# Optimization experiments

Measured on AMD Instinct MI355X. Metric: run time of the kernel, lower is better.

## Reference

```python
import jax, jax.numpy as jnp
import numpy as np

B, T, D, H, DH, FF = 512, 64, 512, 8, 64, 2048
SCALE = DH ** -0.5  # head_dim ** -0.5


def _ln(x, g, b):
    m = x.mean(-1, keepdims=True)
    v = x.var(-1, keepdims=True)
    return (x - m) / jnp.sqrt(v + 1e-5) * g + b


def _l2n(x):
    return x / jnp.maximum(jnp.linalg.norm(x, axis=-1, keepdims=True), 1e-12)


def setup_inputs() -> dict:
    key = jax.random.key(0)
    ks = jax.random.split(key, 16)

    def w(k, shape):
        fan_in = shape[0]
        return jax.random.normal(k, shape, jnp.float32) / np.sqrt(fan_in).astype(np.float32)

    return {
        'item_seq': jax.random.normal(ks[0], (B, T, D), jnp.float32),
        'user_static_emb': jax.random.normal(ks[1], (B, D), jnp.float32),
        'last_item_emb': jax.random.normal(ks[2], (B, D), jnp.float32),
        'init_state': jnp.zeros((B, H, DH, DH), jnp.float32),
        'Wq': w(ks[3], (D, D)), 'Wk': w(ks[4], (D, D)), 'Wv': w(ks[5], (D, D)),
        'Wa': w(ks[6], (D, H)), 'ba': jnp.zeros((H,), jnp.float32),
        'We': w(ks[7], (D, H)), 'be': jnp.zeros((H,), jnp.float32),
        'mcW1': w(ks[8], (2 * D, D)), 'mcb1': jnp.zeros((D,), jnp.float32),
        'mcg': jnp.ones((D,), jnp.float32), 'mcbt': jnp.zeros((D,), jnp.float32),
        'mcW2': w(ks[9], (D, 2 * D + 2 * H)), 'mcb2': jnp.zeros((2 * D + 2 * H,), jnp.float32),
        'Wo': w(ks[10], (D, D)), 'bo': jnp.zeros((D,), jnp.float32),
        'W1': w(ks[11], (D, FF)), 'b1': jnp.zeros((FF,), jnp.float32),
        'W2': w(ks[12], (FF, D)), 'b2': jnp.zeros((D,), jnp.float32),
        'n1g': jnp.ones((D,), jnp.float32), 'n1b': jnp.zeros((D,), jnp.float32),
        'n2g': jnp.ones((D,), jnp.float32), 'n2b': jnp.zeros((D,), jnp.float32),
    }


def reference(item_seq, user_static_emb, last_item_emb, init_state,
              Wq, Wk, Wv, Wa, ba, We, be,
              mcW1, mcb1, mcg, mcbt, mcW2, mcb2,
              Wo, bo, W1, b1, W2, b2, n1g, n1b, n2g, n2b):
    def read(q_emb, state):
        # q: (B,H,Dh) L2-normalized; read = S @ q per head
        q = _l2n((q_emb @ Wq).reshape(-1, H, DH))
        return jnp.einsum('bhij,bhj->bhi', state, q).reshape(-1, D)

    us_norm = _ln(user_static_emb, n1g, n1b)  # constant across steps

    def step(state, item):
        i_norm = _ln(item, n1g, n1b)
        mem_ctx = read(i_norm, state)
        meta_in = jnp.concatenate([us_norm, mem_ctx], axis=-1)
        h = jax.nn.relu(_ln(meta_in @ mcW1 + mcb1, mcg, mcbt))
        mo = h @ mcW2 + mcb2
        gamma, beta = mo[:, :D], mo[:, D:2 * D]
        alpha_bias, eta_bias = mo[:, 2 * D:2 * D + H], mo[:, 2 * D + H:]
        mod = i_norm * (1.0 + jnp.tanh(gamma)) + beta
        k = _l2n((mod @ Wk).reshape(-1, H, DH))
        v = (mod @ Wv).reshape(-1, H, DH)
        alpha = jax.nn.sigmoid(mod @ Wa + ba + alpha_bias)[:, :, None, None]
        eta = (jax.nn.sigmoid(mod @ We + be + eta_bias) * SCALE)[:, :, None, None]
        pred = jnp.einsum('bhij,bhj->bhi', state, k)
        upd = jnp.einsum('bhi,bhj->bhij', v - pred, k)  # rank-1 outer-product write
        return (1.0 - alpha) * state + eta * upd, None

    state, _ = jax.lax.scan(step, init_state, jnp.swapaxes(item_seq, 0, 1))

    # predict (read) path
    q_norm = _ln(last_item_emb, n1g, n1b)
    attn = read(q_norm, state) @ Wo + bo
    x = user_static_emb + attn
    x2 = _ln(x, n2g, n2b)
    ffn = jax.nn.relu(x2 @ W1 + b1) @ W2 + b2
    return x + ffn
```

## Files before the change

kernel.cpp:

```cpp
#include <hip/hip_runtime.h>
#include <cmath>

constexpr int cB = 512, cT = 64, cD = 512, cH = 8, cDH = 64, cFF = 2048;
constexpr float cSCALE = 0.125f;

typedef short bfrag __attribute__((ext_vector_type(8)));
typedef float f32x4 __attribute__((ext_vector_type(4)));

__device__ __forceinline__ short f2bf(float x) {
  union { float f; unsigned u; } v{x};
  unsigned r = v.u + 0x7fff + ((v.u >> 16) & 1);
  return (short)(r >> 16);
}
__device__ __forceinline__ float bf2f(short s) {
  union { unsigned u; float f; } v;
  v.u = ((unsigned)(unsigned short)s) << 16;
  return v.f;
}
__device__ __forceinline__ float sigm(float z) { return 1.f / (1.f + __expf(-z)); }

enum GemmMode { MQ = 0, MWO, MFF1, MFF2 };

struct GemmArgs {
  const float *A, *A2, *sm, *sr, *g, *b;
  const short *WT, *WT2;
  const float *bias, *extra;
  float *O;
  short *Os;
};

template<int MODE>
__device__ __forceinline__ float loadA(const GemmArgs& p, int r, int k) {
  if constexpr (MODE == MQ) {
    int t = r >> 9, bb = r & 511;
    float v = (t < cT) ? p.A[((size_t)bb * cT + t) * cD + k]
                       : p.A2[(size_t)bb * cD + k];
    return (v - p.sm[r]) * p.sr[r] * p.g[k] + p.b[k];
  } else if constexpr (MODE == MFF1) {
    return (p.A[(size_t)r * cD + k] - p.sm[r]) * p.sr[r] * p.g[k] + p.b[k];
  } else if constexpr (MODE == MFF2) {
    return p.A[(size_t)r * cFF + k];
  } else {
    return p.A[(size_t)r * cD + k];
  }
}

template<int MODE>
__device__ __forceinline__ void epi(const GemmArgs& p, int r, int cn, float acc) {
  if constexpr (MODE == MQ) {
    p.Os[(size_t)r * cD + cn] = f2bf(acc);
  } else if constexpr (MODE == MWO) {
    p.O[(size_t)r * cD + cn] = p.extra[(size_t)r * cD + cn] + acc + p.bias[cn];
  } else if constexpr (MODE == MFF1) {
    p.O[(size_t)r * cFF + cn] = fmaxf(acc + p.bias[cn], 0.f);
  } else {
    p.O[(size_t)r * cD + cn] = p.extra[(size_t)r * cD + cn] + acc + p.bias[cn];
  }
}

template<int MODE, int LDW>
__global__ __launch_bounds__(256) void mgemm(GemmArgs p, int K) {
  __shared__ short As[64][32];
  __shared__ short Bs[64][32];
  const int tid = threadIdx.x;
  const int lane = tid & 63, wid = tid >> 6;
  const int wm = wid & 1, wn = wid >> 1;
  const int l15 = lane & 15, qd = lane >> 4;
  const int row0 = blockIdx.x * 64;
  const int n0 = blockIdx.y * 64;

  f32x4 acc[2][2] = {};
  const int sm = tid >> 2;
  const int sk = (tid & 3) * 8;

  for (int k0 = 0; k0 < K; k0 += 32) {
    {
      short tmp[8];
#pragma unroll
      for (int j = 0; j < 8; ++j)
        tmp[j] = f2bf(loadA<MODE>(p, row0 + sm, k0 + sk + j));
      *((bfrag*)&As[sm][0] + (sk >> 3)) = *(bfrag*)tmp;
    }
    *((bfrag*)&Bs[sm][0] + (sk >> 3)) =
        *(const bfrag*)(p.WT + (size_t)(n0 + sm) * LDW + k0 + sk);
    __syncthreads();
    bfrag a0 = *((bfrag*)&As[wm * 32 + l15][0] + qd);
    bfrag a1 = *((bfrag*)&As[wm * 32 + 16 + l15][0] + qd);
    bfrag b0 = *((bfrag*)&Bs[wn * 32 + l15][0] + qd);
    bfrag b1 = *((bfrag*)&Bs[wn * 32 + 16 + l15][0] + qd);
    acc[0][0] = __builtin_amdgcn_mfma_f32_16x16x32_bf16(a0, b0, acc[0][0], 0, 0, 0);
    acc[0][1] = __builtin_amdgcn_mfma_f32_16x16x32_bf16(a0, b1, acc[0][1], 0, 0, 0);
    acc[1][0] = __builtin_amdgcn_mfma_f32_16x16x32_bf16(a1, b0, acc[1][0], 0, 0, 0);
    acc[1][1] = __builtin_amdgcn_mfma_f32_16x16x32_bf16(a1, b1, acc[1][1], 0, 0, 0);
    __syncthreads();
  }

#pragma unroll
  for (int fm = 0; fm < 2; ++fm)
#pragma unroll
    for (int fn = 0; fn < 2; ++fn)
#pragma unroll
      for (int rg = 0; rg < 4; ++rg)
        epi<MODE>(p, row0 + wm * 32 + fm * 16 + qd * 4 + rg,
                  n0 + wn * 32 + fn * 16 + l15, acc[fm][fn][rg]);
}

template<int MODE, int LDW>
__global__ __launch_bounds__(256) void pgemm(GemmArgs p, int K) {
  __shared__ short Ah[64][32], Al[64][32];
  __shared__ short Bh[64][32], Bl[64][32];
  const int tid = threadIdx.x;
  const int lane = tid & 63, wid = tid >> 6;
  const int wm = wid & 1, wn = wid >> 1;
  const int l15 = lane & 15, qd = lane >> 4;
  const int row0 = blockIdx.x * 64;
  const int n0 = blockIdx.y * 64;

  f32x4 acc[2][2] = {};
  const int sm = tid >> 2;
  const int sk = (tid & 3) * 8;

  for (int k0 = 0; k0 < K; k0 += 32) {
    {
      short th[8], tl[8];
#pragma unroll
      for (int j = 0; j < 8; ++j) {
        float a = loadA<MODE>(p, row0 + sm, k0 + sk + j);
        short h = f2bf(a);
        th[j] = h;
        tl[j] = f2bf(a - bf2f(h));
      }
      *((bfrag*)&Ah[sm][0] + (sk >> 3)) = *(bfrag*)th;
      *((bfrag*)&Al[sm][0] + (sk >> 3)) = *(bfrag*)tl;
    }
    *((bfrag*)&Bh[sm][0] + (sk >> 3)) =
        *(const bfrag*)(p.WT + (size_t)(n0 + sm) * LDW + k0 + sk);
    *((bfrag*)&Bl[sm][0] + (sk >> 3)) =
        *(const bfrag*)(p.WT2 + (size_t)(n0 + sm) * LDW + k0 + sk);
    __syncthreads();
#pragma unroll
    for (int fm = 0; fm < 2; ++fm) {
      bfrag ah = *((bfrag*)&Ah[wm * 32 + fm * 16 + l15][0] + qd);
      bfrag al = *((bfrag*)&Al[wm * 32 + fm * 16 + l15][0] + qd);
#pragma unroll
      for (int fn = 0; fn < 2; ++fn) {
        bfrag bh = *((bfrag*)&Bh[wn * 32 + fn * 16 + l15][0] + qd);
        bfrag bl = *((bfrag*)&Bl[wn * 32 + fn * 16 + l15][0] + qd);
        acc[fm][fn] = __builtin_amdgcn_mfma_f32_16x16x32_bf16(al, bh, acc[fm][fn], 0, 0, 0);
        acc[fm][fn] = __builtin_amdgcn_mfma_f32_16x16x32_bf16(ah, bl, acc[fm][fn], 0, 0, 0);
        acc[fm][fn] = __builtin_amdgcn_mfma_f32_16x16x32_bf16(ah, bh, acc[fm][fn], 0, 0, 0);
      }
    }
    __syncthreads();
  }

#pragma unroll
  for (int fm = 0; fm < 2; ++fm)
#pragma unroll
    for (int fn = 0; fn < 2; ++fn)
#pragma unroll
      for (int rg = 0; rg < 4; ++rg)
        epi<MODE>(p, row0 + wm * 32 + fm * 16 + qd * 4 + rg,
                  n0 + wn * 32 + fn * 16 + l15, acc[fm][fn][rg]);
}

__global__ __launch_bounds__(256) void tconv(const float* __restrict__ W,
                                             short* __restrict__ WT, int K, int N) {
  __shared__ float tile[32][33];
  int k0 = blockIdx.x * 32, n0 = blockIdx.y * 32;
  int tx = threadIdx.x & 31, ty = threadIdx.x >> 5;
#pragma unroll
  for (int j = 0; j < 32; j += 8) {
    int k = k0 + ty + j, n = n0 + tx;
    tile[ty + j][tx] = (k < K && n < N) ? W[(size_t)k * N + n] : 0.f;
  }
  __syncthreads();
#pragma unroll
  for (int j = 0; j < 32; j += 8) {
    int n = n0 + ty + j, k = k0 + tx;
    if (n < N && k < K) WT[(size_t)n * K + k] = f2bf(tile[tx][ty + j]);
  }
}

__global__ __launch_bounds__(256) void tconv2(const float* __restrict__ W,
                                              short* __restrict__ WTh,
                                              short* __restrict__ WTl, int K, int N) {
  __shared__ float tile[32][33];
  int k0 = blockIdx.x * 32, n0 = blockIdx.y * 32;
  int tx = threadIdx.x & 31, ty = threadIdx.x >> 5;
#pragma unroll
  for (int j = 0; j < 32; j += 8) {
    int k = k0 + ty + j, n = n0 + tx;
    tile[ty + j][tx] = (k < K && n < N) ? W[(size_t)k * N + n] : 0.f;
  }
  __syncthreads();
#pragma unroll
  for (int j = 0; j < 32; j += 8) {
    int n = n0 + ty + j, k = k0 + tx;
    if (n < N && k < K) {
      float v = tile[tx][ty + j];
      short h = f2bf(v);
      WTh[(size_t)n * K + k] = h;
      WTl[(size_t)n * K + k] = f2bf(v - bf2f(h));
    }
  }
}

__global__ __launch_bounds__(256) void ln_stats_k(
    const float* __restrict__ item_seq, const float* __restrict__ last_item,
    const float* __restrict__ user, const float* __restrict__ n1g,
    const float* __restrict__ n1b, float* __restrict__ lnm,
    float* __restrict__ lnr, float* __restrict__ us_norm) {
  const int lane = threadIdx.x & 63;
  const int w = blockIdx.x * 4 + (threadIdx.x >> 6);
  const float* src;
  int cls, bi = 0;
  if (w < cT * cB) {
    int t = w >> 9, bb = w & 511;
    src = item_seq + ((size_t)bb * cT + t) * cD;
    cls = 0;
  } else if (w < cT * cB + cB) {
    bi = w - cT * cB;
    src = last_item + (size_t)bi * cD;
    cls = 1;
  } else {
    bi = w - cT * cB - cB;
    src = user + (size_t)bi * cD;
    cls = 2;
  }
  float x[8], s = 0.f, ss = 0.f;
#pragma unroll
  for (int i = 0; i < 8; ++i) {
    float v = src[lane + i * 64];
    x[i] = v; s += v; ss += v * v;
  }
#pragma unroll
  for (int o = 32; o >= 1; o >>= 1) { s += __shfl_xor(s, o); ss += __shfl_xor(ss, o); }
  float m = s * (1.f / cD);
  float rstd = rsqrtf(ss * (1.f / cD) - m * m + 1e-5f);
  if (cls == 0) {
    if (lane == 0) { lnm[w] = m; lnr[w] = rstd; }
  } else if (cls == 1) {
    if (lane == 0) { lnm[cT * cB + bi] = m; lnr[cT * cB + bi] = rstd; }
  } else {
#pragma unroll
    for (int i = 0; i < 8; ++i) {
      int d = lane + i * 64;
      us_norm[(size_t)bi * cD + d] = (x[i] - m) * rstd * n1g[d] + n1b[d];
    }
  }
}

__global__ __launch_bounds__(256) void row_stats_k(const float* __restrict__ X,
                                                   float* __restrict__ M,
                                                   float* __restrict__ R) {
  const int lane = threadIdx.x & 63;
  const int w = blockIdx.x * 4 + (threadIdx.x >> 6);
  float s = 0.f, ss = 0.f;
#pragma unroll
  for (int i = 0; i < 8; ++i) {
    float v = X[(size_t)w * cD + lane + i * 64];
    s += v; ss += v * v;
  }
#pragma unroll
  for (int o = 32; o >= 1; o >>= 1) { s += __shfl_xor(s, o); ss += __shfl_xor(ss, o); }
  if (lane == 0) {
    float m = s * (1.f / cD);
    M[w] = m;
    R[w] = rsqrtf(ss * (1.f / cD) - m * m + 1e-5f);
  }
}

struct Scan2Params {
  const float *item_seq, *init_state, *us_norm, *lnm, *lnr, *n1g, *n1b;
  const float *mcb1, *mcg, *mcbt, *mcb2, *ba, *be;
  const short *wt_m1, *wt_m2, *wt_k, *wt_v, *wt_ae, *q_all;
  float *mem_ctx;
};

__device__ __forceinline__ bfrag mk_afrag(const float* xr, int kc, int qd) {
  const float* s = xr + kc * 32 + qd * 8;
  float4 a = *(const float4*)s;
  float4 b = *(const float4*)(s + 4);
  short t[8] = {f2bf(a.x), f2bf(a.y), f2bf(a.z), f2bf(a.w),
                f2bf(b.x), f2bf(b.y), f2bf(b.z), f2bf(b.w)};
  return *(bfrag*)t;
}

__global__ __launch_bounds__(1024, 4) void scan2_k(Scan2Params p) {
  const int tid = threadIdx.x;
  const int lane = tid & 63, w = tid >> 6;
  const int bb = w >> 3, h = w & 7;
  const int l15 = lane & 15, qd = lane >> 4;
  const int b0 = blockIdx.x * 2;

  __shared__ float xcat[2][1024];
  __shared__ float rbuf[2][512];
  __shared__ float x2b[2][512];
  __shared__ float mo[2][1040];
  __shared__ float modv[2][512];
  __shared__ float kvb[2][1024];
  __shared__ float khat[16][64];
  __shared__ float qh[16][64];
  __shared__ float aeta[2][8][2];
  __shared__ float st[2][2], st2[2][2];
  __shared__ float cb1[512], cg[512], cbt[512], cb2[1040];
  __shared__ float cn1g[512], cn1b[512], cba[8], cbe[8];

  if (tid < 512) {
    cb1[tid] = p.mcb1[tid]; cg[tid] = p.mcg[tid]; cbt[tid] = p.mcbt[tid];
    cn1g[tid] = p.n1g[tid]; cn1b[tid] = p.n1b[tid];
  }
  cb2[tid] = p.mcb2[tid];
  if (tid < 16) cb2[1024 + tid] = p.mcb2[1024 + tid];
  if (tid < 8) { cba[tid] = p.ba[tid]; cbe[tid] = p.be[tid]; }
  {
    int row = tid >> 9, c = tid & 511;
    xcat[row][c] = p.us_norm[(size_t)(b0 + row) * cD + c];
  }

  float S[64];
  {
    const float* sp = p.init_state + ((((size_t)(b0 + bb)) * cH + h) * cDH + lane) * cDH;
#pragma unroll
    for (int j = 0; j < 64; j += 4) {
      float4 t4 = *(const float4*)(sp + j);
      S[j] = t4.x; S[j + 1] = t4.y; S[j + 2] = t4.z; S[j + 3] = t4.w;
    }
  }
  float memv;
  {
    float qv = bf2f(p.q_all[(size_t)(b0 + bb) * cD + h * cDH + lane]);
    float qs = qv * qv;
#pragma unroll
    for (int o = 32; o >= 1; o >>= 1) qs += __shfl_xor(qs, o);
    qh[w][lane] = qv / fmaxf(sqrtf(qs), 1e-12f);
    memv = 0.f;
#pragma unroll
    for (int j = 0; j < 64; j += 4) {
      float4 q4 = *(const float4*)&qh[w][j];
      memv += S[j] * q4.x + S[j + 1] * q4.y + S[j + 2] * q4.z + S[j + 3] * q4.w;
    }
    xcat[bb][512 + h * cDH + lane] = memv;
  }
  __syncthreads();

  for (int t = 0; t < cT; ++t) {
    {
      f32x4 a0 = {}, a1 = {};
      const int n0 = w * 16, n1 = (w + 16) * 16;
#pragma unroll 4
      for (int kc = 0; kc < 32; ++kc) {
        bfrag A = {};
        if (l15 < 2) A = mk_afrag(&xcat[l15][0], kc, qd);
        bfrag B0 = *(const bfrag*)(p.wt_m1 + (size_t)(n0 + l15) * 1024 + kc * 32 + qd * 8);
        bfrag B1 = *(const bfrag*)(p.wt_m1 + (size_t)(n1 + l15) * 1024 + kc * 32 + qd * 8);
        a0 = __builtin_amdgcn_mfma_f32_16x16x32_bf16(A, B0, a0, 0, 0, 0);
        a1 = __builtin_amdgcn_mfma_f32_16x16x32_bf16(A, B1, a1, 0, 0, 0);
      }
      if (lane < 16) {
        rbuf[0][n0 + lane] = a0[0] + cb1[n0 + lane];
        rbuf[1][n0 + lane] = a0[1] + cb1[n0 + lane];
        rbuf[0][n1 + lane] = a1[0] + cb1[n1 + lane];
        rbuf[1][n1 + lane] = a1[1] + cb1[n1 + lane];
      }
    }
    __syncthreads();
    if (w < 2) {
      float s = 0.f, ss = 0.f;
#pragma unroll
      for (int i = 0; i < 8; ++i) { float v = rbuf[w][lane + i * 64]; s += v; ss += v * v; }
#pragma unroll
      for (int o = 32; o >= 1; o >>= 1) { s += __shfl_xor(s, o); ss += __shfl_xor(ss, o); }
      if (lane == 0) {
        float m = s * (1.f / cD);
        st[w][0] = m;
        st[w][1] = rsqrtf(ss * (1.f / cD) - m * m + 1e-5f);
      }
    } else if (w == 2 && lane < 2) {
      st2[lane][0] = p.lnm[t * cB + b0 + lane];
      st2[lane][1] = p.lnr[t * cB + b0 + lane];
    }
    __syncthreads();
    {
      int row = tid >> 9, c = tid & 511;
      x2b[row][c] = fmaxf((rbuf[row][c] - st[row][0]) * st[row][1] * cg[c] + cbt[c], 0.f);
    }
    __syncthreads();
    {
      f32x4 acc[4] = {};
#pragma unroll 2
      for (int kc = 0; kc < 16; ++kc) {
        bfrag A = {};
        if (l15 < 2) A = mk_afrag(&x2b[l15][0], kc, qd);
#pragma unroll
        for (int tI = 0; tI < 4; ++tI) {
          int n0 = (tI * 16 + w) * 16;
          bfrag B = *(const bfrag*)(p.wt_m2 + (size_t)(n0 + l15) * 512 + kc * 32 + qd * 8);
          acc[tI] = __builtin_amdgcn_mfma_f32_16x16x32_bf16(A, B, acc[tI], 0, 0, 0);
        }
      }
      if (lane < 16)
#pragma unroll
        for (int tI = 0; tI < 4; ++tI) {
          int n0 = (tI * 16 + w) * 16;
          mo[0][n0 + lane] = acc[tI][0] + cb2[n0 + lane];
          mo[1][n0 + lane] = acc[tI][1] + cb2[n0 + lane];
        }
      if (w == 0) {
        f32x4 e = {};
        for (int kc = 0; kc < 16; ++kc) {
          bfrag A = {};
          if (l15 < 2) A = mk_afrag(&x2b[l15][0], kc, qd);
          bfrag B = *(const bfrag*)(p.wt_m2 + (size_t)(1024 + l15) * 512 + kc * 32 + qd * 8);
          e = __builtin_amdgcn_mfma_f32_16x16x32_bf16(A, B, e, 0, 0, 0);
        }
        if (lane < 16) {
          mo[0][1024 + lane] = e[0] + cb2[1024 + lane];
          mo[1][1024 + lane] = e[1] + cb2[1024 + lane];
        }
      }
    }
    __syncthreads();
    {
      int row = tid >> 9, c = tid & 511;
      float inm = (p.item_seq[(((size_t)(b0 + row)) * cT + t) * cD + c] - st2[row][0]) *
                      st2[row][1] * cn1g[c] + cn1b[c];
      modv[row][c] = inm * (1.f + tanhf(mo[row][c])) + mo[row][512 + c];
    }
    __syncthreads();
    {
      f32x4 acc[4] = {};
#pragma unroll 2
      for (int kc = 0; kc < 16; ++kc) {
        bfrag A = {};
        if (l15 < 2) A = mk_afrag(&modv[l15][0], kc, qd);
#pragma unroll
        for (int tI = 0; tI < 4; ++tI) {
          int tile = tI * 16 + w;
          const short* wt = (tile < 32) ? p.wt_k : p.wt_v;
          int n0 = ((tile < 32) ? tile : tile - 32) * 16;
          bfrag B = *(const bfrag*)(wt + (size_t)(n0 + l15) * 512 + kc * 32 + qd * 8);
          acc[tI] = __builtin_amdgcn_mfma_f32_16x16x32_bf16(A, B, acc[tI], 0, 0, 0);
        }
      }
      if (lane < 16)
#pragma unroll
        for (int tI = 0; tI < 4; ++tI) {
          int tile = tI * 16 + w;
          int dst = (tile < 32) ? tile * 16 + lane : 512 + (tile - 32) * 16 + lane;
          kvb[0][dst] = acc[tI][0];
          kvb[1][dst] = acc[tI][1];
        }
      if (w == 0) {
        f32x4 e = {};
        for (int kc = 0; kc < 16; ++kc) {
          bfrag A = {};
          if (l15 < 2) A = mk_afrag(&modv[l15][0], kc, qd);
          bfrag B = *(const bfrag*)(p.wt_ae + (size_t)l15 * 512 + kc * 32 + qd * 8);
          e = __builtin_amdgcn_mfma_f32_16x16x32_bf16(A, B, e, 0, 0, 0);
        }
        if (lane < 16) {
          if (lane < 8) {
            int hh = lane;
            aeta[0][hh][0] = sigm(e[0] + cba[hh] + mo[0][1024 + hh]);
            aeta[1][hh][0] = sigm(e[1] + cba[hh] + mo[1][1024 + hh]);
          } else {
            int hh = lane - 8;
            aeta[0][hh][1] = cSCALE * sigm(e[0] + cbe[hh] + mo[0][1032 + hh]);
            aeta[1][hh][1] = cSCALE * sigm(e[1] + cbe[hh] + mo[1][1032 + hh]);
          }
        }
      }
    }
    __syncthreads();
    {
      float kvv = kvb[bb][h * cDH + lane];
      float ks = kvv * kvv;
#pragma unroll
      for (int o = 32; o >= 1; o >>= 1) ks += __shfl_xor(ks, o);
      khat[w][lane] = kvv / fmaxf(sqrtf(ks), 1e-12f);
      float qv = bf2f(p.q_all[((size_t)(t + 1) * cB + (b0 + bb)) * cD + h * cDH + lane]);
      float qs = qv * qv;
#pragma unroll
      for (int o = 32; o >= 1; o >>= 1) qs += __shfl_xor(qs, o);
      qh[w][lane] = qv / fmaxf(sqrtf(qs), 1e-12f);

      float vv = kvb[bb][512 + h * cDH + lane];
      float al = aeta[bb][h][0], et = aeta[bb][h][1];
      float pred = 0.f;
#pragma unroll
      for (int j = 0; j < 64; j += 4) {
        float4 k4 = *(const float4*)&khat[w][j];
        pred += S[j] * k4.x + S[j + 1] * k4.y + S[j + 2] * k4.z + S[j + 3] * k4.w;
      }
      float f = et * (vv - pred), oma = 1.f - al;
      memv = 0.f;
#pragma unroll
      for (int j = 0; j < 64; j += 4) {
        float4 k4 = *(const float4*)&khat[w][j];
        float4 q4 = *(const float4*)&qh[w][j];
        S[j]     = oma * S[j]     + f * k4.x; memv += S[j]     * q4.x;
        S[j + 1] = oma * S[j + 1] + f * k4.y; memv += S[j + 1] * q4.y;
        S[j + 2] = oma * S[j + 2] + f * k4.z; memv += S[j + 2] * q4.z;
        S[j + 3] = oma * S[j + 3] + f * k4.w; memv += S[j + 3] * q4.w;
      }
      xcat[bb][512 + h * cDH + lane] = memv;
    }
    __syncthreads();
  }

  p.mem_ctx[(size_t)(b0 + bb) * cD + h * cDH + lane] = memv;
}

extern "C" void kernel_launch(void* const* d_in, const int* in_sizes, int n_in,
                              void* d_out, int out_size, void* d_ws, size_t ws_size,
                              hipStream_t stream) {
  (void)in_sizes; (void)n_in; (void)out_size;
  const float* item_seq   = (const float*)d_in[0];
  const float* user_stat  = (const float*)d_in[1];
  const float* last_item  = (const float*)d_in[2];
  const float* init_state = (const float*)d_in[3];
  const float* Wq  = (const float*)d_in[4];
  const float* Wk  = (const float*)d_in[5];
  const float* Wv  = (const float*)d_in[6];
  const float* Wa  = (const float*)d_in[7];
  const float* ba  = (const float*)d_in[8];
  const float* We  = (const float*)d_in[9];
  const float* be  = (const float*)d_in[10];
  const float* mcW1 = (const float*)d_in[11];
  const float* mcb1 = (const float*)d_in[12];
  const float* mcg  = (const float*)d_in[13];
  const float* mcbt = (const float*)d_in[14];
  const float* mcW2 = (const float*)d_in[15];
  const float* mcb2 = (const float*)d_in[16];
  const float* Wo  = (const float*)d_in[17];
  const float* bo  = (const float*)d_in[18];
  const float* W1  = (const float*)d_in[19];
  const float* b1  = (const float*)d_in[20];
  const float* W2  = (const float*)d_in[21];
  const float* b2  = (const float*)d_in[22];
  const float* n1g = (const float*)d_in[23];
  const float* n1b = (const float*)d_in[24];
  const float* n2g = (const float*)d_in[25];
  const float* n2b = (const float*)d_in[26];

  float* ws = (float*)d_ws;
  size_t off = 0;
  auto alloc = [&](size_t n) { float* p = ws + off; off += n; return p; };
  auto salloc = [&](size_t n) { return (short*)alloc((n + 1) / 2); };

  short* q_all   = salloc((size_t)(cT + 1) * cB * cD);
  float* lnm     = alloc((size_t)(cT + 1) * cB);
  float* lnr     = alloc((size_t)(cT + 1) * cB);
  float* us_norm = alloc((size_t)cB * cD);
  float* mem_ctx = alloc((size_t)cB * cD);
  float* x_buf   = alloc((size_t)cB * cD);
  float* xm      = alloc(cB);
  float* xr      = alloc(cB);
  float* u_buf   = alloc((size_t)cB * cFF);
  short* wt_q    = salloc((size_t)512 * 512);
  short* wt_m1   = salloc((size_t)512 * 1024);
  short* wt_m2   = salloc((size_t)1040 * 512);
  short* wt_k    = salloc((size_t)512 * 512);
  short* wt_v    = salloc((size_t)512 * 512);
  short* wt_ae   = salloc((size_t)16 * 512);
  short* wt_o    = salloc((size_t)512 * 512);
  short* wt_o_l  = salloc((size_t)512 * 512);
  short* wt_1    = salloc((size_t)2048 * 512);
  short* wt_1_l  = salloc((size_t)2048 * 512);
  short* wt_2    = salloc((size_t)512 * 2048);
  short* wt_2_l  = salloc((size_t)512 * 2048);
  if (ws_size < off * sizeof(float)) return;

  tconv<<<dim3(16, 16), 256, 0, stream>>>(Wq, wt_q, 512, 512);
  tconv<<<dim3(32, 16), 256, 0, stream>>>(mcW1, wt_m1, 1024, 512);
  tconv<<<dim3(16, 33), 256, 0, stream>>>(mcW2, wt_m2, 512, 1040);
  tconv<<<dim3(16, 16), 256, 0, stream>>>(Wk, wt_k, 512, 512);
  tconv<<<dim3(16, 16), 256, 0, stream>>>(Wv, wt_v, 512, 512);
  tconv<<<dim3(16, 1), 256, 0, stream>>>(Wa, wt_ae, 512, 8);
  tconv<<<dim3(16, 1), 256, 0, stream>>>(We, wt_ae + (size_t)8 * 512, 512, 8);
  tconv2<<<dim3(16, 16), 256, 0, stream>>>(Wo, wt_o, wt_o_l, 512, 512);
  tconv2<<<dim3(16, 64), 256, 0, stream>>>(W1, wt_1, wt_1_l, 512, 2048);
  tconv2<<<dim3(64, 16), 256, 0, stream>>>(W2, wt_2, wt_2_l, 2048, 512);

  ln_stats_k<<<(cT * cB + 2 * cB) / 4, 256, 0, stream>>>(
      item_seq, last_item, user_stat, n1g, n1b, lnm, lnr, us_norm);

  {
    GemmArgs p{}; p.A = item_seq; p.A2 = last_item; p.sm = lnm; p.sr = lnr;
    p.g = n1g; p.b = n1b; p.WT = wt_q; p.Os = q_all;
    mgemm<MQ, 512><<<dim3(520, 8), 256, 0, stream>>>(p, 512);
  }

  {
    Scan2Params sp{};
    sp.item_seq = item_seq; sp.init_state = init_state; sp.us_norm = us_norm;
    sp.lnm = lnm; sp.lnr = lnr; sp.n1g = n1g; sp.n1b = n1b;
    sp.mcb1 = mcb1; sp.mcg = mcg; sp.mcbt = mcbt; sp.mcb2 = mcb2;
    sp.ba = ba; sp.be = be;
    sp.wt_m1 = wt_m1; sp.wt_m2 = wt_m2; sp.wt_k = wt_k; sp.wt_v = wt_v;
    sp.wt_ae = wt_ae; sp.q_all = q_all;
    sp.mem_ctx = mem_ctx;
    scan2_k<<<dim3(cB / 2), dim3(1024), 0, stream>>>(sp);
  }

  {
    GemmArgs p{}; p.A = mem_ctx; p.WT = wt_o; p.WT2 = wt_o_l;
    p.bias = bo; p.extra = user_stat; p.O = x_buf;
    pgemm<MWO, 512><<<dim3(8, 8), 256, 0, stream>>>(p, 512);
  }
  row_stats_k<<<cB / 4, 256, 0, stream>>>(x_buf, xm, xr);
  {
    GemmArgs p{}; p.A = x_buf; p.sm = xm; p.sr = xr; p.g = n2g; p.b = n2b;
    p.WT = wt_1; p.WT2 = wt_1_l; p.bias = b1; p.O = u_buf;
    pgemm<MFF1, 512><<<dim3(8, 32), 256, 0, stream>>>(p, 512);
  }
  {
    GemmArgs p{}; p.A = u_buf; p.WT = wt_2; p.WT2 = wt_2_l;
    p.bias = b2; p.extra = x_buf; p.O = (float*)d_out;
    pgemm<MFF2, 2048><<<dim3(8, 8), 256, 0, stream>>>(p, 2048);
  }
}
```

Before: 7.086 ms.

## Process one batch row per block in scan kernel with bf16 staged activations

```diff
diff --git a/kernel.cpp b/kernel.cpp
--- a/kernel.cpp
+++ b/kernel.cpp
@@ -271,57 +271,46 @@
   }
 }
 
-struct Scan2Params {
+struct Scan3Params {
   const float *item_seq, *init_state, *us_norm, *lnm, *lnr, *n1g, *n1b;
   const float *mcb1, *mcg, *mcbt, *mcb2, *ba, *be;
   const short *wt_m1, *wt_m2, *wt_k, *wt_v, *wt_ae, *q_all;
   float *mem_ctx;
 };
 
-__device__ __forceinline__ bfrag mk_afrag(const float* xr, int kc, int qd) {
-  const float* s = xr + kc * 32 + qd * 8;
-  float4 a = *(const float4*)s;
-  float4 b = *(const float4*)(s + 4);
-  short t[8] = {f2bf(a.x), f2bf(a.y), f2bf(a.z), f2bf(a.w),
-                f2bf(b.x), f2bf(b.y), f2bf(b.z), f2bf(b.w)};
-  return *(bfrag*)t;
-}
-
-__global__ __launch_bounds__(1024, 4) void scan2_k(Scan2Params p) {
+__global__ __launch_bounds__(512, 4) void scan3_k(Scan3Params p) {
   const int tid = threadIdx.x;
   const int lane = tid & 63, w = tid >> 6;
-  const int bb = w >> 3, h = w & 7;
   const int l15 = lane & 15, qd = lane >> 4;
-  const int b0 = blockIdx.x * 2;
-
-  __shared__ float xcat[2][1024];
-  __shared__ float rbuf[2][512];
-  __shared__ float x2b[2][512];
-  __shared__ float mo[2][1040];
-  __shared__ float modv[2][512];
-  __shared__ float kvb[2][1024];
-  __shared__ float khat[16][64];
-  __shared__ float qh[16][64];
-  __shared__ float aeta[2][8][2];
-  __shared__ float st[2][2], st2[2][2];
+  const int b = blockIdx.x;
+
+  __shared__ float xcat[1024];
+  __shared__ short abf[1024];
+  __shared__ short azero[32];
+  __shared__ float rbuf[512];
+  __shared__ float mo[1040];
+  __shared__ float kvb[1024];
+  __shared__ float khat[8][64];
+  __shared__ float qhat[8][64];
+  __shared__ float aeta[8][2];
+  __shared__ float st[2], st2[2];
+  __shared__ float pfi_s[512];
+  __shared__ short pfq_s[512];
   __shared__ float cb1[512], cg[512], cbt[512], cb2[1040];
   __shared__ float cn1g[512], cn1b[512], cba[8], cbe[8];
 
-  if (tid < 512) {
-    cb1[tid] = p.mcb1[tid]; cg[tid] = p.mcg[tid]; cbt[tid] = p.mcbt[tid];
-    cn1g[tid] = p.n1g[tid]; cn1b[tid] = p.n1b[tid];
-  }
+  cb1[tid] = p.mcb1[tid]; cg[tid] = p.mcg[tid]; cbt[tid] = p.mcbt[tid];
+  cn1g[tid] = p.n1g[tid]; cn1b[tid] = p.n1b[tid];
   cb2[tid] = p.mcb2[tid];
+  cb2[512 + tid] = p.mcb2[512 + tid];
   if (tid < 16) cb2[1024 + tid] = p.mcb2[1024 + tid];
   if (tid < 8) { cba[tid] = p.ba[tid]; cbe[tid] = p.be[tid]; }
-  {
-    int row = tid >> 9, c = tid & 511;
-    xcat[row][c] = p.us_norm[(size_t)(b0 + row) * cD + c];
-  }
+  if (tid < 32) azero[tid] = 0;
+  xcat[tid] = p.us_norm[(size_t)b * cD + tid];
 
   float S[64];
   {
-    const float* sp = p.init_state + ((((size_t)(b0 + bb)) * cH + h) * cDH + lane) * cDH;
+    const float* sp = p.init_state + (((size_t)b * cH + w) * cDH + lane) * cDH;
 #pragma unroll
     for (int j = 0; j < 64; j += 4) {
       float4 t4 = *(const float4*)(sp + j);
@@ -330,164 +319,172 @@
   }
   float memv;
   {
-    float qv = bf2f(p.q_all[(size_t)(b0 + bb) * cD + h * cDH + lane]);
+    float qv = bf2f(p.q_all[(size_t)b * cD + w * cDH + lane]);
     float qs = qv * qv;
 #pragma unroll
     for (int o = 32; o >= 1; o >>= 1) qs += __shfl_xor(qs, o);
-    qh[w][lane] = qv / fmaxf(sqrtf(qs), 1e-12f);
+    qhat[w][lane] = qv / fmaxf(sqrtf(qs), 1e-12f);
     memv = 0.f;
 #pragma unroll
     for (int j = 0; j < 64; j += 4) {
-      float4 q4 = *(const float4*)&qh[w][j];
+      float4 q4 = *(const float4*)&qhat[w][j];
       memv += S[j] * q4.x + S[j + 1] * q4.y + S[j + 2] * q4.z + S[j + 3] * q4.w;
     }
-    xcat[bb][512 + h * cDH + lane] = memv;
+    xcat[512 + w * cDH + lane] = memv;
   }
   __syncthreads();
 
   for (int t = 0; t < cT; ++t) {
+    float pfi = p.item_seq[((size_t)b * cT + t) * cD + tid];
+    short pfq = p.q_all[((size_t)(t + 1) * cB + b) * cD + tid];
+    float pst2m = 0.f, pst2r = 0.f;
+    if (tid == 0) { pst2m = p.lnm[t * cB + b]; pst2r = p.lnr[t * cB + b]; }
+    abf[tid] = f2bf(xcat[tid]);
+    abf[512 + tid] = f2bf(xcat[512 + tid]);
+    __syncthreads();
+
     {
-      f32x4 a0 = {}, a1 = {};
-      const int n0 = w * 16, n1 = (w + 16) * 16;
-#pragma unroll 4
+      f32x4 acc[4] = {};
+#pragma unroll 2
       for (int kc = 0; kc < 32; ++kc) {
-        bfrag A = {};
-        if (l15 < 2) A = mk_afrag(&xcat[l15][0], kc, qd);
-        bfrag B0 = *(const bfrag*)(p.wt_m1 + (size_t)(n0 + l15) * 1024 + kc * 32 + qd * 8);
-        bfrag B1 = *(const bfrag*)(p.wt_m1 + (size_t)(n1 + l15) * 1024 + kc * 32 + qd * 8);
-        a0 = __builtin_amdgcn_mfma_f32_16x16x32_bf16(A, B0, a0, 0, 0, 0);
-        a1 = __builtin_amdgcn_mfma_f32_16x16x32_bf16(A, B1, a1, 0, 0, 0);
-      }
-      if (lane < 16) {
-        rbuf[0][n0 + lane] = a0[0] + cb1[n0 + lane];
-        rbuf[1][n0 + lane] = a0[1] + cb1[n0 + lane];
-        rbuf[0][n1 + lane] = a1[0] + cb1[n1 + lane];
-        rbuf[1][n1 + lane] = a1[1] + cb1[n1 + lane];
-      }
-    }
-    __syncthreads();
-    if (w < 2) {
+        const short* ap = (l15 == 0) ? &abf[kc * 32 + qd * 8] : &azero[qd * 8];
+        bfrag A = *(const bfrag*)ap;
+#pragma unroll
+        for (int ti = 0; ti < 4; ++ti) {
+          int n0 = (w + ti * 8) * 16;
+          bfrag B = *(const bfrag*)(p.wt_m1 + (size_t)(n0 + l15) * 1024 + kc * 32 + qd * 8);
+          acc[ti] = __builtin_amdgcn_mfma_f32_16x16x32_bf16(A, B, acc[ti], 0, 0, 0);
+        }
+      }
+      if (lane < 16)
+#pragma unroll
+        for (int ti = 0; ti < 4; ++ti) {
+          int n0 = (w + ti * 8) * 16;
+          rbuf[n0 + lane] = acc[ti][0] + cb1[n0 + lane];
+        }
+    }
+    pfi_s[tid] = pfi;
+    pfq_s[tid] = pfq;
+    if (tid == 0) { st2[0] = pst2m; st2[1] = pst2r; }
+    __syncthreads();
+
+    if (w == 0) {
       float s = 0.f, ss = 0.f;
 #pragma unroll
-      for (int i = 0; i < 8; ++i) { float v = rbuf[w][lane + i * 64]; s += v; ss += v * v; }
+      for (int i = 0; i < 8; ++i) { float v = rbuf[lane + i * 64]; s += v; ss += v * v; }
 #pragma unroll
       for (int o = 32; o >= 1; o >>= 1) { s += __shfl_xor(s, o); ss += __shfl_xor(ss, o); }
       if (lane == 0) {
         float m = s * (1.f / cD);
-        st[w][0] = m;
-        st[w][1] = rsqrtf(ss * (1.f / cD) - m * m + 1e-5f);
-      }
-    } else if (w == 2 && lane < 2) {
-      st2[lane][0] = p.lnm[t * cB + b0 + lane];
-      st2[lane][1] = p.lnr[t * cB + b0 + lane];
-    }
-    __syncthreads();
+        st[0] = m;
+        st[1] = rsqrtf(ss * (1.f / cD) - m * m + 1e-5f);
+      }
+    }
+    __syncthreads();
+
+    abf[tid] = f2bf(fmaxf((rbuf[tid] - st[0]) * st[1] * cg[tid] + cbt[tid], 0.f));
+    __syncthreads();
+
     {
-      int row = tid >> 9, c = tid & 511;
-      x2b[row][c] = fmaxf((rbuf[row][c] - st[row][0]) * st[row][1] * cg[c] + cbt[c], 0.f);
-    }
-    __syncthreads();
-    {
-      f32x4 acc[4] = {};
+#pragma unroll
+      for (int g = 0; g < 2; ++g) {
+        f32x4 acc[4] = {};
 #pragma unroll 2
-      for (int kc = 0; kc < 16; ++kc) {
-        bfrag A = {};
-        if (l15 < 2) A = mk_afrag(&x2b[l15][0], kc, qd);
-#pragma unroll
-        for (int tI = 0; tI < 4; ++tI) {
-          int n0 = (tI * 16 + w) * 16;
-          bfrag B = *(const bfrag*)(p.wt_m2 + (size_t)(n0 + l15) * 512 + kc * 32 + qd * 8);
-          acc[tI] = __builtin_amdgcn_mfma_f32_16x16x32_bf16(A, B, acc[tI], 0, 0, 0);
+        for (int kc = 0; kc < 16; ++kc) {
+          const short* ap = (l15 == 0) ? &abf[kc * 32 + qd * 8] : &azero[qd * 8];
+          bfrag A = *(const bfrag*)ap;
+#pragma unroll
+          for (int ti = 0; ti < 4; ++ti) {
+            int n0 = (w + (g * 4 + ti) * 8) * 16;
+            bfrag B = *(const bfrag*)(p.wt_m2 + (size_t)(n0 + l15) * 512 + kc * 32 + qd * 8);
+            acc[ti] = __builtin_amdgcn_mfma_f32_16x16x32_bf16(A, B, acc[ti], 0, 0, 0);
+          }
         }
-      }
-      if (lane < 16)
-#pragma unroll
-        for (int tI = 0; tI < 4; ++tI) {
-          int n0 = (tI * 16 + w) * 16;
-          mo[0][n0 + lane] = acc[tI][0] + cb2[n0 + lane];
-          mo[1][n0 + lane] = acc[tI][1] + cb2[n0 + lane];
-        }
+        if (lane < 16)
+#pragma unroll
+          for (int ti = 0; ti < 4; ++ti) {
+            int n0 = (w + (g * 4 + ti) * 8) * 16;
+            mo[n0 + lane] = acc[ti][0] + cb2[n0 + lane];
+          }
+      }
       if (w == 0) {
         f32x4 e = {};
         for (int kc = 0; kc < 16; ++kc) {
-          bfrag A = {};
-          if (l15 < 2) A = mk_afrag(&x2b[l15][0], kc, qd);
+          const short* ap = (l15 == 0) ? &abf[kc * 32 + qd * 8] : &azero[qd * 8];
+          bfrag A = *(const bfrag*)ap;
           bfrag B = *(const bfrag*)(p.wt_m2 + (size_t)(1024 + l15) * 512 + kc * 32 + qd * 8);
           e = __builtin_amdgcn_mfma_f32_16x16x32_bf16(A, B, e, 0, 0, 0);
         }
-        if (lane < 16) {
-          mo[0][1024 + lane] = e[0] + cb2[1024 + lane];
-          mo[1][1024 + lane] = e[1] + cb2[1024 + lane];
+        if (lane < 16) mo[1024 + lane] = e[0] + cb2[1024 + lane];
+      }
+    }
+    __syncthreads();
+
+    {
+      float inm = (pfi_s[tid] - st2[0]) * st2[1] * cn1g[tid] + cn1b[tid];
+      abf[tid] = f2bf(inm * (1.f + tanhf(mo[tid])) + mo[512 + tid]);
+    }
+    __syncthreads();
+
+    {
+#pragma unroll
+      for (int g = 0; g < 2; ++g) {
+        f32x4 acc[4] = {};
+#pragma unroll 2
+        for (int kc = 0; kc < 16; ++kc) {
+          const short* ap = (l15 == 0) ? &abf[kc * 32 + qd * 8] : &azero[qd * 8];
+          bfrag A = *(const bfrag*)ap;
+#pragma unroll
+          for (int ti = 0; ti < 4; ++ti) {
+            int tile = w + (g * 4 + ti) * 8;
+            const short* wt = (tile < 32) ? p.wt_k : p.wt_v;
+            int n0 = ((tile < 32) ? tile : tile - 32) * 16;
+            bfrag B = *(const bfrag*)(wt + (size_t)(n0 + l15) * 512 + kc * 32 + qd * 8);
+            acc[ti] = __builtin_amdgcn_mfma_f32_16x16x32_bf16(A, B, acc[ti], 0, 0, 0);
+          }
         }
-      }
-    }
-    __syncthreads();
-    {
-      int row = tid >> 9, c = tid & 511;
-      float inm = (p.item_seq[(((size_t)(b0 + row)) * cT + t) * cD + c] - st2[row][0]) *
-                      st2[row][1] * cn1g[c] + cn1b[c];
-      modv[row][c] = inm * (1.f + tanhf(mo[row][c])) + mo[row][512 + c];
-    }
-    __syncthreads();
-    {
-      f32x4 acc[4] = {};
-#pragma unroll 2
-      for (int kc = 0; kc < 16; ++kc) {
-        bfrag A = {};
-        if (l15 < 2) A = mk_afrag(&modv[l15][0], kc, qd);
-#pragma unroll
-        for (int tI = 0; tI < 4; ++tI) {
-          int tile = tI * 16 + w;
-          const short* wt = (tile < 32) ? p.wt_k : p.wt_v;
-          int n0 = ((tile < 32) ? tile : tile - 32) * 16;
-          bfrag B = *(const bfrag*)(wt + (size_t)(n0 + l15) * 512 + kc * 32 + qd * 8);
-          acc[tI] = __builtin_amdgcn_mfma_f32_16x16x32_bf16(A, B, acc[tI], 0, 0, 0);
-        }
-      }
-      if (lane < 16)
-#pragma unroll
-        for (int tI = 0; tI < 4; ++tI) {
-          int tile = tI * 16 + w;
-          int dst = (tile < 32) ? tile * 16 + lane : 512 + (tile - 32) * 16 + lane;
-          kvb[0][dst] = acc[tI][0];
-          kvb[1][dst] = acc[tI][1];
-        }
+        if (lane < 16)
+#pragma unroll
+          for (int ti = 0; ti < 4; ++ti) {
+            int tile = w + (g * 4 + ti) * 8;
+            int dst = (tile < 32) ? tile * 16 + lane : 512 + (tile - 32) * 16 + lane;
+            kvb[dst] = acc[ti][0];
+          }
+      }
       if (w == 0) {
         f32x4 e = {};
         for (int kc = 0; kc < 16; ++kc) {
-          bfrag A = {};
-          if (l15 < 2) A = mk_afrag(&modv[l15][0], kc, qd);
+          const short* ap = (l15 == 0) ? &abf[kc * 32 + qd * 8] : &azero[qd * 8];
+          bfrag A = *(const bfrag*)ap;
           bfrag B = *(const bfrag*)(p.wt_ae + (size_t)l15 * 512 + kc * 32 + qd * 8);
           e = __builtin_amdgcn_mfma_f32_16x16x32_bf16(A, B, e, 0, 0, 0);
         }
         if (lane < 16) {
           if (lane < 8) {
-            int hh = lane;
-            aeta[0][hh][0] = sigm(e[0] + cba[hh] + mo[0][1024 + hh]);
-            aeta[1][hh][0] = sigm(e[1] + cba[hh] + mo[1][1024 + hh]);
+            aeta[lane][0] = sigm(e[0] + cba[lane] + mo[1024 + lane]);
           } else {
             int hh = lane - 8;
-            aeta[0][hh][1] = cSCALE * sigm(e[0] + cbe[hh] + mo[0][1032 + hh]);
-            aeta[1][hh][1] = cSCALE * sigm(e[1] + cbe[hh] + mo[1][1032 + hh]);
+            aeta[hh][1] = cSCALE * sigm(e[0] + cbe[hh] + mo[1032 + hh]);
           }
         }
       }
     }
     __syncthreads();
+
     {
-      float kvv = kvb[bb][h * cDH + lane];
+      float kvv = kvb[w * cDH + lane];
       float ks = kvv * kvv;
 #pragma unroll
       for (int o = 32; o >= 1; o >>= 1) ks += __shfl_xor(ks, o);
       khat[w][lane] = kvv / fmaxf(sqrtf(ks), 1e-12f);
-      float qv = bf2f(p.q_all[((size_t)(t + 1) * cB + (b0 + bb)) * cD + h * cDH + lane]);
+      float qv = bf2f(pfq_s[w * cDH + lane]);
       float qs = qv * qv;
 #pragma unroll
       for (int o = 32; o >= 1; o >>= 1) qs += __shfl_xor(qs, o);
-      qh[w][lane] = qv / fmaxf(sqrtf(qs), 1e-12f);
-
-      float vv = kvb[bb][512 + h * cDH + lane];
-      float al = aeta[bb][h][0], et = aeta[bb][h][1];
+      qhat[w][lane] = qv / fmaxf(sqrtf(qs), 1e-12f);
+
+      float vv = kvb[512 + w * cDH + lane];
+      float al = aeta[w][0], et = aeta[w][1];
       float pred = 0.f;
 #pragma unroll
       for (int j = 0; j < 64; j += 4) {
@@ -499,18 +496,18 @@
 #pragma unroll
       for (int j = 0; j < 64; j += 4) {
         float4 k4 = *(const float4*)&khat[w][j];
-        float4 q4 = *(const float4*)&qh[w][j];
+        float4 q4 = *(const float4*)&qhat[w][j];
         S[j]     = oma * S[j]     + f * k4.x; memv += S[j]     * q4.x;
         S[j + 1] = oma * S[j + 1] + f * k4.y; memv += S[j + 1] * q4.y;
         S[j + 2] = oma * S[j + 2] + f * k4.z; memv += S[j + 2] * q4.z;
         S[j + 3] = oma * S[j + 3] + f * k4.w; memv += S[j + 3] * q4.w;
       }
-      xcat[bb][512 + h * cDH + lane] = memv;
-    }
-    __syncthreads();
-  }
-
-  p.mem_ctx[(size_t)(b0 + bb) * cD + h * cDH + lane] = memv;
+      xcat[512 + w * cDH + lane] = memv;
+    }
+    __syncthreads();
+  }
+
+  p.mem_ctx[(size_t)b * cD + w * cDH + lane] = memv;
 }
 
 extern "C" void kernel_launch(void* const* d_in, const int* in_sizes, int n_in,
@@ -594,7 +591,7 @@
   }
 
   {
-    Scan2Params sp{};
+    Scan3Params sp{};
     sp.item_seq = item_seq; sp.init_state = init_state; sp.us_norm = us_norm;
     sp.lnm = lnm; sp.lnr = lnr; sp.n1g = n1g; sp.n1b = n1b;
     sp.mcb1 = mcb1; sp.mcg = mcg; sp.mcbt = mcbt; sp.mcb2 = mcb2;
@@ -602,7 +599,7 @@
     sp.wt_m1 = wt_m1; sp.wt_m2 = wt_m2; sp.wt_k = wt_k; sp.wt_v = wt_v;
     sp.wt_ae = wt_ae; sp.q_all = q_all;
     sp.mem_ctx = mem_ctx;
-    scan2_k<<<dim3(cB / 2), dim3(1024), 0, stream>>>(sp);
+    scan3_k<<<dim3(cB), dim3(512), 0, stream>>>(sp);
   }
 
   {
```

Measured after the change: 12.30 ms. +73.6%, slower.
